# Optimization experiments

Hardware: AMD Instinct MI355X
Metric: run time of the kernel (lower is better)

The kernel has to match this reference:

```python
import jax, jax.numpy as jnp
import numpy as np

B, D, M = 1024, 4096, 128          # batch, input_dim, output_dim (num modules)
HS = [32, 64, 128, 256, 512]       # hidden_dims


def setup_inputs() -> dict:
    key = jax.random.key(0)
    ks = jax.random.split(key, 12)
    inp = {}
    inp["x"] = jax.random.normal(ks[0], (B, D), dtype=jnp.float32)
    # first dense layer: Linear(input_dim, hidden_dims[0]*output_dim)
    inp["W0"] = jax.random.normal(ks[1], (HS[0] * M, D), dtype=jnp.float32) / np.float32(np.sqrt(D))
    inp["b0"] = jnp.zeros((HS[0] * M,), jnp.float32)
    # block-diagonal MaskedLinear layers stored as per-module blocks [M, h_out, h_in]
    for i in range(len(HS) - 1):
        inp[f"W{i+1}"] = jax.random.normal(ks[2 + i], (M, HS[i + 1], HS[i]), dtype=jnp.float32) / np.float32(np.sqrt(HS[i]))
        inp[f"b{i+1}"] = jnp.zeros((M, HS[i + 1]), jnp.float32)
    # output MaskedLinear(h_last, 1, M): blocks [M, 1, h_last] stored as [M, h_last]
    inp["Wout"] = jax.random.normal(ks[10], (M, HS[-1]), dtype=jnp.float32) / np.float32(np.sqrt(HS[-1]))
    inp["bout"] = jnp.zeros((M,), jnp.float32)
    return inp


def reference(x, W0, b0, W1, b1, W2, b2, W3, b3, W4, b4, Wout, bout):
    # Dropout is inference-disabled; MaskedLinear's block-diagonal dense GEMM is
    # computed exactly as a grouped GEMM over the M module blocks (same math,
    # skipping the structurally-zero off-diagonal blocks).
    h = jax.nn.relu(x @ W0.T + b0)                 # [B, M*h0]
    h = h.reshape(x.shape[0], M, HS[0])            # [B, M, h0]
    for W, b in ((W1, b1), (W2, b2), (W3, b3), (W4, b4)):
        h = jax.nn.relu(jnp.einsum('bmi,moi->bmo', h, W) + b)  # [B, M, h_out]
    logits = jnp.einsum('bmi,mi->bm', h, Wout) + bout          # [B, M]
    return jax.nn.sigmoid(logits)
```

## Files before the change

kernel.cpp:

```cpp
#include <hip/hip_runtime.h>
#include <hip/hip_bf16.h>


using bf16 = __hip_bfloat16;
typedef short bf16x8 __attribute__((ext_vector_type(8)));
typedef float f32x4 __attribute__((ext_vector_type(4)));

constexpr int B_ = 1024;
constexpr int M_ = 128;

#define WAITV(N) asm volatile("s_waitcnt vmcnt(" #N ")" ::: "memory")
#define WAITL()  asm volatile("s_waitcnt lgkmcnt(0)" ::: "memory")
#define BAR()    asm volatile("s_barrier" ::: "memory")

__device__ __forceinline__ void gload16_lds(const bf16* gp, bf16* lp) {
    __builtin_amdgcn_global_load_lds(
        (__attribute__((address_space(1))) void*)const_cast<bf16*>(gp),
        (__attribute__((address_space(3))) void*)lp,
        16, 0, 0);
}

struct CvtArgs {
    const float4* src[6];
    short4* dst[6];
};
__global__ void cvt_all(CvtArgs a) {
    constexpr int starts[7] = {0, 1048576, 5242880, 5308416, 5570560,
                               6619136, 10813440};
    int i = blockIdx.x * blockDim.x + threadIdx.x;
    if (i >= starts[6]) return;
    int s = 0;
#pragma unroll
    for (int k = 1; k < 6; ++k) s += (i >= starts[k]) ? 1 : 0;
    int off = i - starts[s];
    float4 v = a.src[s][off];
    union { bf16 h[4]; short4 s4; } u;
    u.h[0] = __float2bfloat16(v.x);
    u.h[1] = __float2bfloat16(v.y);
    u.h[2] = __float2bfloat16(v.z);
    u.h[3] = __float2bfloat16(v.w);
    a.dst[s][off] = u.s4;
}

__global__ __launch_bounds__(256, 2)
void gemm_l0(const bf16* __restrict__ A, const bf16* __restrict__ W,
             const float* __restrict__ bias, bf16* __restrict__ C) {
    constexpr int LDA = 4096;
    __shared__ __align__(16) bf16 sA[2][2][128 * 32];
    __shared__ __align__(16) bf16 sB[2][2][64 * 32];

    const int tid = threadIdx.x, w = tid >> 6, lane = tid & 63;
    const int q = lane >> 4, ln = lane & 15;
    const int lr = lane >> 2, lk = lane & 3;
    const int swz = (lk ^ (lr & 3)) * 8;
    const int wm = w >> 1, wn = w & 1;
    const int r0 = blockIdx.y * 128, c0 = blockIdx.x * 64;

    auto stage = [&](int s, int set) {
        const int k0 = s * 64;
#pragma unroll
        for (int h = 0; h < 2; ++h) {
#pragma unroll
            for (int t = 0; t < 2; ++t) {
                int grp = w * 2 + t;
                gload16_lds(A + (size_t)(r0 + grp * 16 + lr) * LDA + k0 + h * 32 + swz,
                            &sA[set][h][grp * 512]);
            }
            gload16_lds(W + (size_t)(c0 + w * 16 + lr) * LDA + k0 + h * 32 + swz,
                        &sB[set][h][w * 512]);
        }
    };

    f32x4 acc[4][2];
#pragma unroll
    for (int i = 0; i < 4; ++i)
#pragma unroll
        for (int j = 0; j < 2; ++j) acc[i][j] = (f32x4){0.f, 0.f, 0.f, 0.f};

    stage(0, 0);
    stage(1, 1);
    for (int r = 0; r < 64; ++r) {
        if (r < 63) WAITV(6); else WAITV(0);
        BAR();
        const int set = r & 1;
        bf16x8 aF[2][4], bF[2][2];
#pragma unroll
        for (int h = 0; h < 2; ++h) {
#pragma unroll
            for (int i = 0; i < 4; ++i) {
                int row = wm * 64 + i * 16 + ln;
                aF[h][i] = *(const bf16x8*)&sA[set][h][row * 32 + ((q ^ (row & 3)) * 8)];
            }
#pragma unroll
            for (int j = 0; j < 2; ++j) {
                int rn = wn * 32 + j * 16 + ln;
                bF[h][j] = *(const bf16x8*)&sB[set][h][rn * 32 + ((q ^ (rn & 3)) * 8)];
            }
        }
        WAITL();
        BAR();
        if (r + 2 < 64) stage(r + 2, set);
#pragma unroll
        for (int h = 0; h < 2; ++h)
#pragma unroll
            for (int i = 0; i < 4; ++i)
#pragma unroll
                for (int j = 0; j < 2; ++j)
                    acc[i][j] = __builtin_amdgcn_mfma_f32_16x16x32_bf16(
                        aF[h][i], bF[h][j], acc[i][j], 0, 0, 0);
    }

#pragma unroll
    for (int j = 0; j < 2; ++j) {
        int col = c0 + wn * 32 + j * 16 + ln;
        float bv = bias[col];
#pragma unroll
        for (int i = 0; i < 4; ++i)
#pragma unroll
            for (int rr = 0; rr < 4; ++rr) {
                int row = r0 + wm * 64 + i * 16 + q * 4 + rr;
                float v = acc[i][j][rr] + bv;
                v = v > 0.f ? v : 0.f;
                C[(size_t)row * 4096 + col] = __float2bfloat16(v);
            }
    }
}

__global__ __launch_bounds__(256, 2)
void modules_fused(const bf16* __restrict__ h0g,
                   const bf16* __restrict__ W1b, const float* __restrict__ b1,
                   const bf16* __restrict__ W2b, const float* __restrict__ b2,
                   const bf16* __restrict__ W3b, const float* __restrict__ b3,
                   const bf16* __restrict__ W4b, const float* __restrict__ b4,
                   const float* __restrict__ Wout, const float* __restrict__ bout,
                   float* __restrict__ out) {
    constexpr int H3O = 0, H2O = 16896, H1O = 25600, H0O = 30208;
    constexpr int P4B0 = 16896, P4B1 = 20992, P4B2 = 25600;
    __shared__ __align__(16) bf16 pool[32768];

    const int tid = threadIdx.x, w = tid >> 6, lane = tid & 63;
    const int q = lane >> 4, ln = lane & 15;
    const int lr = lane >> 2, lk = lane & 3;
    const int swz = (lk ^ (lr & 3)) * 8;
    const int m = blockIdx.y;
    const int r0 = blockIdx.x * 64;

    const bf16* W1m = W1b + (size_t)m * 64 * 32;
    const bf16* W2m = W2b + (size_t)m * 128 * 64;
    const bf16* W3m = W3b + (size_t)m * 256 * 128;
    const bf16* W4m = W4b + (size_t)m * 512 * 256;

    auto stage = [&](const bf16* G, int ldg, int rows, int nr0, int k0, int woff) {
#pragma unroll
        for (int t = 0; t < rows / 64; ++t) {
            int r = t * 64 + w * 16 + lr;
            gload16_lds(G + (size_t)(nr0 + r) * ldg + k0 + swz,
                        pool + woff + t * 2048 + w * 512);
        }
    };
    auto rdA = [&](int hoff, int stride, int row, int kc) -> bf16x8 {
        return *(const bf16x8*)&pool[hoff + row * stride + kc * 8];
    };
    auto rdA0 = [&](int row) -> bf16x8 {
        return *(const bf16x8*)&pool[H0O + row * 32 + ((q ^ (row & 3)) * 8)];
    };
    auto rdB = [&](int woff, int rn) -> bf16x8 {
        return *(const bf16x8*)&pool[woff + rn * 32 + ((q ^ (rn & 3)) * 8)];
    };
    auto wrH = [&](int hoff, int stride, int row, int col, float v) {
        pool[hoff + row * stride + col] = __float2bfloat16(v);
    };

    float b1v = b1[m * 64 + w * 16 + ln];
    float b2v[2], b3v[4], b4v[4][2], wov[4][2];
#pragma unroll
    for (int j = 0; j < 2; ++j) b2v[j] = b2[m * 128 + w * 32 + j * 16 + ln];
#pragma unroll
    for (int j = 0; j < 4; ++j) b3v[j] = b3[m * 256 + w * 64 + j * 16 + ln];
#pragma unroll
    for (int nc = 0; nc < 4; ++nc)
#pragma unroll
        for (int j = 0; j < 2; ++j) {
            int col = nc * 128 + w * 32 + j * 16 + ln;
            b4v[nc][j] = b4[(size_t)m * 512 + col];
            wov[nc][j] = Wout[(size_t)m * 512 + col];
        }
    float boutv = bout[m];
    WAITV(0);

    gload16_lds(h0g + (size_t)(r0 + w * 16 + lr) * 4096 + m * 32 + swz,
                pool + H0O + w * 512);
    stage(W1m, 32, 64, 0, 0, 8192);
    stage(W2m, 64, 128, 0, 0, 0);
    stage(W2m, 64, 128, 0, 32, 4096);

    WAITV(4);
    BAR();
    {
        bf16x8 aF[4], bF;
#pragma unroll
        for (int i = 0; i < 4; ++i) aF[i] = rdA0(i * 16 + ln);
        bF = rdB(8192, w * 16 + ln);
        WAITL();
        BAR();
        f32x4 a1[4];
#pragma unroll
        for (int i = 0; i < 4; ++i) {
            a1[i] = (f32x4){0.f, 0.f, 0.f, 0.f};
            a1[i] = __builtin_amdgcn_mfma_f32_16x16x32_bf16(aF[i], bF, a1[i], 0, 0, 0);
        }
        int col = w * 16 + ln;
#pragma unroll
        for (int i = 0; i < 4; ++i)
#pragma unroll
            for (int rr = 0; rr < 4; ++rr) {
                float v = a1[i][rr] + b1v;
                v = v > 0.f ? v : 0.f;
                wrH(H1O, 72, i * 16 + q * 4 + rr, col, v);
            }
        WAITL();
        BAR();
    }

    {
        f32x4 a2[4][2];
#pragma unroll
        for (int i = 0; i < 4; ++i)
#pragma unroll
            for (int j = 0; j < 2; ++j) a2[i][j] = (f32x4){0.f, 0.f, 0.f, 0.f};
#pragma unroll
        for (int kr = 0; kr < 2; ++kr) {
            if (kr == 0) WAITV(2); else WAITV(0);
            BAR();
            bf16x8 aF[4], bF[2];
#pragma unroll
            for (int i = 0; i < 4; ++i) aF[i] = rdA(H1O, 72, i * 16 + ln, kr * 4 + q);
#pragma unroll
            for (int j = 0; j < 2; ++j) bF[j] = rdB(kr * 4096, w * 32 + j * 16 + ln);
            WAITL();
            BAR();
            if (kr == 1) {
                stage(W3m, 128, 256, 0, 0, 0);
                stage(W3m, 128, 256, 0, 32, 8192);
            }
#pragma unroll
            for (int i = 0; i < 4; ++i)
#pragma unroll
                for (int j = 0; j < 2; ++j)
                    a2[i][j] = __builtin_amdgcn_mfma_f32_16x16x32_bf16(aF[i], bF[j], a2[i][j], 0, 0, 0);
        }
#pragma unroll
        for (int j = 0; j < 2; ++j) {
            int col = w * 32 + j * 16 + ln;
#pragma unroll
            for (int i = 0; i < 4; ++i)
#pragma unroll
                for (int rr = 0; rr < 4; ++rr) {
                    float v = a2[i][j][rr] + b2v[j];
                    v = v > 0.f ? v : 0.f;
                    wrH(H2O, 136, i * 16 + q * 4 + rr, col, v);
                }
        }
        WAITL();
        BAR();
    }

    {
        f32x4 a3[4][4];
#pragma unroll
        for (int i = 0; i < 4; ++i)
#pragma unroll
            for (int j = 0; j < 4; ++j) a3[i][j] = (f32x4){0.f, 0.f, 0.f, 0.f};
#pragma unroll
        for (int kr = 0; kr < 4; ++kr) {
            if (kr < 3) WAITV(4); else WAITV(0);
            BAR();
            bf16x8 aF[4], bF[4];
#pragma unroll
            for (int i = 0; i < 4; ++i) aF[i] = rdA(H2O, 136, i * 16 + ln, kr * 4 + q);
#pragma unroll
            for (int j = 0; j < 4; ++j) bF[j] = rdB((kr & 1) * 8192, w * 64 + j * 16 + ln);
            WAITL();
            BAR();
            if (kr == 0)      stage(W3m, 128, 256, 0, 64, 0);
            else if (kr == 1) stage(W3m, 128, 256, 0, 96, 8192);
            else if (kr == 3) {
                stage(W4m, 256, 128, 0, 0, P4B0);
                stage(W4m, 256, 128, 0, 32, P4B1);
            }
#pragma unroll
            for (int i = 0; i < 4; ++i)
#pragma unroll
                for (int j = 0; j < 4; ++j)
                    a3[i][j] = __builtin_amdgcn_mfma_f32_16x16x32_bf16(aF[i], bF[j], a3[i][j], 0, 0, 0);
        }
#pragma unroll
        for (int j = 0; j < 4; ++j) {
            int col = w * 64 + j * 16 + ln;
#pragma unroll
            for (int i = 0; i < 4; ++i)
#pragma unroll
                for (int rr = 0; rr < 4; ++rr) {
                    float v = a3[i][j][rr] + b3v[j];
                    v = v > 0.f ? v : 0.f;
                    wrH(H3O, 264, i * 16 + q * 4 + rr, col, v);
                }
        }
        WAITL();
        BAR();
    }

    float pl[4][4];
#pragma unroll
    for (int i = 0; i < 4; ++i)
#pragma unroll
        for (int rr = 0; rr < 4; ++rr) pl[i][rr] = 0.f;

#pragma unroll
    for (int nc = 0; nc < 4; ++nc) {
        f32x4 a4[4][2];
#pragma unroll
        for (int i = 0; i < 4; ++i)
#pragma unroll
            for (int j = 0; j < 2; ++j) a4[i][j] = (f32x4){0.f, 0.f, 0.f, 0.f};
#pragma unroll
        for (int kr = 0; kr < 8; ++kr) {
            const int r = nc * 8 + kr;
            if (r + 2 < 32) {
                const int r2 = r + 2;
                const int wb2 = (r2 % 3 == 0) ? P4B0 : (r2 % 3 == 1) ? P4B1 : P4B2;
                stage(W4m, 256, 128, (r2 >> 3) * 128, (r2 & 7) * 32, wb2);
            }
            if (r < 30) WAITV(4); else if (r == 30) WAITV(2); else WAITV(0);
            BAR();
            const int wb = (r % 3 == 0) ? P4B0 : (r % 3 == 1) ? P4B1 : P4B2;
            bf16x8 aF[4], bF[2];
#pragma unroll
            for (int i = 0; i < 4; ++i) aF[i] = rdA(H3O, 264, i * 16 + ln, kr * 4 + q);
#pragma unroll
            for (int j = 0; j < 2; ++j) bF[j] = rdB(wb, w * 32 + j * 16 + ln);
            WAITL();
            BAR();
#pragma unroll
            for (int i = 0; i < 4; ++i)
#pragma unroll
                for (int j = 0; j < 2; ++j)
                    a4[i][j] = __builtin_amdgcn_mfma_f32_16x16x32_bf16(aF[i], bF[j], a4[i][j], 0, 0, 0);
        }
#pragma unroll
        for (int j = 0; j < 2; ++j) {
            float bb = b4v[nc][j], wv = wov[nc][j];
#pragma unroll
            for (int i = 0; i < 4; ++i)
#pragma unroll
                for (int rr = 0; rr < 4; ++rr) {
                    float v = a4[i][j][rr] + bb;
                    v = v > 0.f ? v : 0.f;
                    pl[i][rr] += v * wv;
                }
        }
    }

    float* sc = (float*)&pool[H0O];
#pragma unroll
    for (int i = 0; i < 4; ++i)
#pragma unroll
        for (int rr = 0; rr < 4; ++rr) {
            float p = pl[i][rr];
            p += __shfl_xor(p, 1);
            p += __shfl_xor(p, 2);
            p += __shfl_xor(p, 4);
            p += __shfl_xor(p, 8);
            if (ln == 0) sc[w * 64 + i * 16 + q * 4 + rr] = p;
        }
    __syncthreads();
    if (tid < 64) {
        float s = sc[tid] + sc[64 + tid] + sc[128 + tid] + sc[192 + tid];
        float lg = s + boutv;
        out[(size_t)(r0 + tid) * M_ + m] = 1.f / (1.f + __expf(-lg));
    }
}

extern "C" void kernel_launch(void* const* d_in, const int* in_sizes, int n_in,
                              void* d_out, int out_size, void* d_ws, size_t ws_size,
                              hipStream_t stream) {
    const float* x    = (const float*)d_in[0];
    const float* W0   = (const float*)d_in[1];
    const float* b0   = (const float*)d_in[2];
    const float* W1   = (const float*)d_in[3];
    const float* b1   = (const float*)d_in[4];
    const float* W2   = (const float*)d_in[5];
    const float* b2   = (const float*)d_in[6];
    const float* W3   = (const float*)d_in[7];
    const float* b3   = (const float*)d_in[8];
    const float* W4   = (const float*)d_in[9];
    const float* b4   = (const float*)d_in[10];
    const float* Wout = (const float*)d_in[11];
    const float* bout = (const float*)d_in[12];
    float* out = (float*)d_out;

    char* ws = (char*)d_ws;
    size_t off = 0;
    auto alloc = [&](size_t bytes) -> void* {
        off = (off + 255) & ~(size_t)255;
        void* p = ws + off;
        off += bytes;
        return p;
    };
    bf16* W0b = (bf16*)alloc((size_t)4096 * 4096 * 2);
    bf16* W1b = (bf16*)alloc((size_t)M_ * 64 * 32 * 2);
    bf16* W2b = (bf16*)alloc((size_t)M_ * 128 * 64 * 2);
    bf16* W3b = (bf16*)alloc((size_t)M_ * 256 * 128 * 2);
    bf16* W4b = (bf16*)alloc((size_t)M_ * 512 * 256 * 2);
    bf16* xb  = (bf16*)alloc((size_t)B_ * 4096 * 2);
    bf16* h0  = (bf16*)alloc((size_t)B_ * 4096 * 2);

    CvtArgs ca;
    ca.src[0] = (const float4*)x;  ca.dst[0] = (short4*)xb;
    ca.src[1] = (const float4*)W0; ca.dst[1] = (short4*)W0b;
    ca.src[2] = (const float4*)W1; ca.dst[2] = (short4*)W1b;
    ca.src[3] = (const float4*)W2; ca.dst[3] = (short4*)W2b;
    ca.src[4] = (const float4*)W3; ca.dst[4] = (short4*)W3b;
    ca.src[5] = (const float4*)W4; ca.dst[5] = (short4*)W4b;
    cvt_all<<<(10813440 + 255) / 256, 256, 0, stream>>>(ca);

    {
        dim3 g(4096 / 64, B_ / 128, 1);
        gemm_l0<<<g, 256, 0, stream>>>(xb, W0b, b0, h0);
    }
    {
        dim3 g(B_ / 64, M_, 1);
        modules_fused<<<g, 256, 0, stream>>>(h0, W1b, b1, W2b, b2, W3b, b3,
                                             W4b, b4, Wout, bout, out);
    }
}
```

Before: 321.9 us.

## Load module weights directly into registers and shrink LDS for higher occupancy

Weight fragments for layers 1-4 are now loaded from global memory straight into registers with a two-deep register prefetch, replacing the LDS staging and its per-step barriers. Activations stay in LDS with an XOR swizzle in place of padded strides, and the layer-3 output is computed in two column halves. These changes cut LDS from 64KB to 48KB and raise launch bounds to 3 blocks per CU. The aim is fewer barriers and more resident waves, at the cost of uncoalesced per-lane global weight loads, more register pressure, and exposed global latency.

```diff
diff --git a/kernel.cpp b/kernel.cpp
--- a/kernel.cpp
+++ b/kernel.cpp
@@ -126,7 +126,7 @@
     }
 }
 
-__global__ __launch_bounds__(256, 2)
+__global__ __launch_bounds__(256, 3)
 void modules_fused(const bf16* __restrict__ h0g,
                    const bf16* __restrict__ W1b, const float* __restrict__ b1,
                    const bf16* __restrict__ W2b, const float* __restrict__ b2,
@@ -134,9 +134,8 @@
                    const bf16* __restrict__ W4b, const float* __restrict__ b4,
                    const float* __restrict__ Wout, const float* __restrict__ bout,
                    float* __restrict__ out) {
-    constexpr int H3O = 0, H2O = 16896, H1O = 25600, H0O = 30208;
-    constexpr int P4B0 = 16896, P4B1 = 20992, P4B2 = 25600;
-    __shared__ __align__(16) bf16 pool[32768];
+    constexpr int H3 = 0, H1 = 0, H0 = 4096, H2 = 16384;
+    __shared__ __align__(16) bf16 pool[24576];
 
     const int tid = threadIdx.x, w = tid >> 6, lane = tid & 63;
     const int q = lane >> 4, ln = lane & 15;
@@ -150,33 +149,29 @@
     const bf16* W3m = W3b + (size_t)m * 256 * 128;
     const bf16* W4m = W4b + (size_t)m * 512 * 256;
 
-    auto stage = [&](const bf16* G, int ldg, int rows, int nr0, int k0, int woff) {
-#pragma unroll
-        for (int t = 0; t < rows / 64; ++t) {
-            int r = t * 64 + w * 16 + lr;
-            gload16_lds(G + (size_t)(nr0 + r) * ldg + k0 + swz,
-                        pool + woff + t * 2048 + w * 512);
-        }
-    };
-    auto rdA = [&](int hoff, int stride, int row, int kc) -> bf16x8 {
-        return *(const bf16x8*)&pool[hoff + row * stride + kc * 8];
+    auto rdX = [&](int base, int nch, int row, int chunk) -> bf16x8 {
+        return *(const bf16x8*)&pool[base + row * nch * 8 + ((chunk ^ (row & 7)) * 8)];
     };
     auto rdA0 = [&](int row) -> bf16x8 {
-        return *(const bf16x8*)&pool[H0O + row * 32 + ((q ^ (row & 3)) * 8)];
-    };
-    auto rdB = [&](int woff, int rn) -> bf16x8 {
-        return *(const bf16x8*)&pool[woff + rn * 32 + ((q ^ (rn & 3)) * 8)];
-    };
-    auto wrH = [&](int hoff, int stride, int row, int col, float v) {
-        pool[hoff + row * stride + col] = __float2bfloat16(v);
+        return *(const bf16x8*)&pool[H0 + row * 32 + ((q ^ (row & 3)) * 8)];
+    };
+    auto wrX = [&](int base, int nch, int row, int col, float v) {
+        pool[base + row * nch * 8 + (((col >> 3) ^ (row & 7)) * 8) + (col & 7)] =
+            __float2bfloat16(v);
+    };
+    auto ldW = [&](const bf16* Wm, int ldg, int row, int kc) -> bf16x8 {
+        return *(const bf16x8*)&Wm[(size_t)row * ldg + kc * 8];
     };
 
     float b1v = b1[m * 64 + w * 16 + ln];
-    float b2v[2], b3v[4], b4v[4][2], wov[4][2];
+    float b2v[2], b3v[2][2], b4v[4][2], wov[4][2];
 #pragma unroll
     for (int j = 0; j < 2; ++j) b2v[j] = b2[m * 128 + w * 32 + j * 16 + ln];
 #pragma unroll
-    for (int j = 0; j < 4; ++j) b3v[j] = b3[m * 256 + w * 64 + j * 16 + ln];
+    for (int oc = 0; oc < 2; ++oc)
+#pragma unroll
+        for (int j = 0; j < 2; ++j)
+            b3v[oc][j] = b3[m * 256 + oc * 128 + w * 32 + j * 16 + ln];
 #pragma unroll
     for (int nc = 0; nc < 4; ++nc)
 #pragma unroll
@@ -186,129 +181,123 @@
             wov[nc][j] = Wout[(size_t)m * 512 + col];
         }
     float boutv = bout[m];
+
+    gload16_lds(h0g + (size_t)(r0 + w * 16 + lr) * 4096 + m * 32 + swz,
+                pool + H0 + w * 512);
+    bf16x8 f1 = ldW(W1m, 32, w * 16 + ln, q);
+    bf16x8 f2[2][2], f3[2][2], f4[2][2];
+#pragma unroll
+    for (int kk = 0; kk < 2; ++kk)
+#pragma unroll
+        for (int j = 0; j < 2; ++j)
+            f2[kk][j] = ldW(W2m, 64, w * 32 + j * 16 + ln, kk * 4 + q);
+#pragma unroll
+    for (int p = 0; p < 2; ++p)
+#pragma unroll
+        for (int j = 0; j < 2; ++j)
+            f3[p][j] = ldW(W3m, 128, w * 32 + j * 16 + ln, p * 4 + q);
     WAITV(0);
-
-    gload16_lds(h0g + (size_t)(r0 + w * 16 + lr) * 4096 + m * 32 + swz,
-                pool + H0O + w * 512);
-    stage(W1m, 32, 64, 0, 0, 8192);
-    stage(W2m, 64, 128, 0, 0, 0);
-    stage(W2m, 64, 128, 0, 32, 4096);
-
-    WAITV(4);
     BAR();
+
     {
-        bf16x8 aF[4], bF;
-#pragma unroll
-        for (int i = 0; i < 4; ++i) aF[i] = rdA0(i * 16 + ln);
-        bF = rdB(8192, w * 16 + ln);
+        f32x4 a1[4];
+#pragma unroll
+        for (int i = 0; i < 4; ++i) {
+            a1[i] = (f32x4){0.f, 0.f, 0.f, 0.f};
+            a1[i] = __builtin_amdgcn_mfma_f32_16x16x32_bf16(rdA0(i * 16 + ln), f1,
+                                                            a1[i], 0, 0, 0);
+        }
+#pragma unroll
+        for (int i = 0; i < 4; ++i)
+#pragma unroll
+            for (int rr = 0; rr < 4; ++rr) {
+                float v = a1[i][rr] + b1v;
+                wrX(H1, 8, i * 16 + q * 4 + rr, w * 16 + ln, v > 0.f ? v : 0.f);
+            }
         WAITL();
         BAR();
-        f32x4 a1[4];
-#pragma unroll
-        for (int i = 0; i < 4; ++i) {
-            a1[i] = (f32x4){0.f, 0.f, 0.f, 0.f};
-            a1[i] = __builtin_amdgcn_mfma_f32_16x16x32_bf16(aF[i], bF, a1[i], 0, 0, 0);
-        }
-        int col = w * 16 + ln;
+    }
+
+    {
+        f32x4 a2[4][2];
 #pragma unroll
         for (int i = 0; i < 4; ++i)
 #pragma unroll
-            for (int rr = 0; rr < 4; ++rr) {
-                float v = a1[i][rr] + b1v;
-                v = v > 0.f ? v : 0.f;
-                wrH(H1O, 72, i * 16 + q * 4 + rr, col, v);
-            }
+            for (int j = 0; j < 2; ++j) a2[i][j] = (f32x4){0.f, 0.f, 0.f, 0.f};
+#pragma unroll
+        for (int kk = 0; kk < 2; ++kk) {
+            bf16x8 aF[4];
+#pragma unroll
+            for (int i = 0; i < 4; ++i) aF[i] = rdX(H1, 8, i * 16 + ln, kk * 4 + q);
+#pragma unroll
+            for (int i = 0; i < 4; ++i)
+#pragma unroll
+                for (int j = 0; j < 2; ++j)
+                    a2[i][j] = __builtin_amdgcn_mfma_f32_16x16x32_bf16(
+                        aF[i], f2[kk][j], a2[i][j], 0, 0, 0);
+        }
+#pragma unroll
+        for (int j = 0; j < 2; ++j)
+#pragma unroll
+            for (int i = 0; i < 4; ++i)
+#pragma unroll
+                for (int rr = 0; rr < 4; ++rr) {
+                    float v = a2[i][j][rr] + b2v[j];
+                    wrX(H2, 16, i * 16 + q * 4 + rr, w * 32 + j * 16 + ln,
+                        v > 0.f ? v : 0.f);
+                }
         WAITL();
         BAR();
     }
 
-    {
-        f32x4 a2[4][2];
+#pragma unroll
+    for (int oc = 0; oc < 2; ++oc) {
+        f32x4 a3[4][2];
 #pragma unroll
         for (int i = 0; i < 4; ++i)
 #pragma unroll
-            for (int j = 0; j < 2; ++j) a2[i][j] = (f32x4){0.f, 0.f, 0.f, 0.f};
-#pragma unroll
-        for (int kr = 0; kr < 2; ++kr) {
-            if (kr == 0) WAITV(2); else WAITV(0);
-            BAR();
-            bf16x8 aF[4], bF[2];
-#pragma unroll
-            for (int i = 0; i < 4; ++i) aF[i] = rdA(H1O, 72, i * 16 + ln, kr * 4 + q);
-#pragma unroll
-            for (int j = 0; j < 2; ++j) bF[j] = rdB(kr * 4096, w * 32 + j * 16 + ln);
-            WAITL();
-            BAR();
-            if (kr == 1) {
-                stage(W3m, 128, 256, 0, 0, 0);
-                stage(W3m, 128, 256, 0, 32, 8192);
-            }
+            for (int j = 0; j < 2; ++j) a3[i][j] = (f32x4){0.f, 0.f, 0.f, 0.f};
+#pragma unroll
+        for (int kr = 0; kr < 4; ++kr) {
+            const int r = oc * 4 + kr, p = r & 1;
+            bf16x8 c0 = f3[p][0], c1 = f3[p][1];
+            if (r + 2 < 8) {
+                const int r2 = r + 2;
+#pragma unroll
+                for (int j = 0; j < 2; ++j)
+                    f3[p][j] = ldW(W3m, 128,
+                                   (r2 >> 2) * 128 + w * 32 + j * 16 + ln,
+                                   (r2 & 3) * 4 + q);
+            }
+            bf16x8 aF[4];
+#pragma unroll
+            for (int i = 0; i < 4; ++i) aF[i] = rdX(H2, 16, i * 16 + ln, kr * 4 + q);
+#pragma unroll
+            for (int i = 0; i < 4; ++i) {
+                a3[i][0] = __builtin_amdgcn_mfma_f32_16x16x32_bf16(aF[i], c0,
+                                                                   a3[i][0], 0, 0, 0);
+                a3[i][1] = __builtin_amdgcn_mfma_f32_16x16x32_bf16(aF[i], c1,
+                                                                   a3[i][1], 0, 0, 0);
+            }
+        }
+#pragma unroll
+        for (int j = 0; j < 2; ++j)
 #pragma unroll
             for (int i = 0; i < 4; ++i)
 #pragma unroll
-                for (int j = 0; j < 2; ++j)
-                    a2[i][j] = __builtin_amdgcn_mfma_f32_16x16x32_bf16(aF[i], bF[j], a2[i][j], 0, 0, 0);
-        }
-#pragma unroll
-        for (int j = 0; j < 2; ++j) {
-            int col = w * 32 + j * 16 + ln;
-#pragma unroll
-            for (int i = 0; i < 4; ++i)
-#pragma unroll
                 for (int rr = 0; rr < 4; ++rr) {
-                    float v = a2[i][j][rr] + b2v[j];
-                    v = v > 0.f ? v : 0.f;
-                    wrH(H2O, 136, i * 16 + q * 4 + rr, col, v);
+                    float v = a3[i][j][rr] + b3v[oc][j];
+                    wrX(H3, 32, i * 16 + q * 4 + rr,
+                        oc * 128 + w * 32 + j * 16 + ln, v > 0.f ? v : 0.f);
                 }
-        }
-        WAITL();
-        BAR();
-    }
-
-    {
-        f32x4 a3[4][4];
-#pragma unroll
-        for (int i = 0; i < 4; ++i)
-#pragma unroll
-            for (int j = 0; j < 4; ++j) a3[i][j] = (f32x4){0.f, 0.f, 0.f, 0.f};
-#pragma unroll
-        for (int kr = 0; kr < 4; ++kr) {
-            if (kr < 3) WAITV(4); else WAITV(0);
-            BAR();
-            bf16x8 aF[4], bF[4];
-#pragma unroll
-            for (int i = 0; i < 4; ++i) aF[i] = rdA(H2O, 136, i * 16 + ln, kr * 4 + q);
-#pragma unroll
-            for (int j = 0; j < 4; ++j) bF[j] = rdB((kr & 1) * 8192, w * 64 + j * 16 + ln);
-            WAITL();
-            BAR();
-            if (kr == 0)      stage(W3m, 128, 256, 0, 64, 0);
-            else if (kr == 1) stage(W3m, 128, 256, 0, 96, 8192);
-            else if (kr == 3) {
-                stage(W4m, 256, 128, 0, 0, P4B0);
-                stage(W4m, 256, 128, 0, 32, P4B1);
-            }
-#pragma unroll
-            for (int i = 0; i < 4; ++i)
-#pragma unroll
-                for (int j = 0; j < 4; ++j)
-                    a3[i][j] = __builtin_amdgcn_mfma_f32_16x16x32_bf16(aF[i], bF[j], a3[i][j], 0, 0, 0);
-        }
-#pragma unroll
-        for (int j = 0; j < 4; ++j) {
-            int col = w * 64 + j * 16 + ln;
-#pragma unroll
-            for (int i = 0; i < 4; ++i)
-#pragma unroll
-                for (int rr = 0; rr < 4; ++rr) {
-                    float v = a3[i][j][rr] + b3v[j];
-                    v = v > 0.f ? v : 0.f;
-                    wrH(H3O, 264, i * 16 + q * 4 + rr, col, v);
-                }
-        }
-        WAITL();
-        BAR();
-    }
+    }
+#pragma unroll
+    for (int p = 0; p < 2; ++p)
+#pragma unroll
+        for (int j = 0; j < 2; ++j)
+            f4[p][j] = ldW(W4m, 256, w * 32 + j * 16 + ln, p * 4 + q);
+    WAITL();
+    BAR();
 
     float pl[4][4];
 #pragma unroll
@@ -325,27 +314,26 @@
             for (int j = 0; j < 2; ++j) a4[i][j] = (f32x4){0.f, 0.f, 0.f, 0.f};
 #pragma unroll
         for (int kr = 0; kr < 8; ++kr) {
-            const int r = nc * 8 + kr;
+            const int r = nc * 8 + kr, p = r & 1;
+            bf16x8 c0 = f4[p][0], c1 = f4[p][1];
             if (r + 2 < 32) {
                 const int r2 = r + 2;
-                const int wb2 = (r2 % 3 == 0) ? P4B0 : (r2 % 3 == 1) ? P4B1 : P4B2;
-                stage(W4m, 256, 128, (r2 >> 3) * 128, (r2 & 7) * 32, wb2);
-            }
-            if (r < 30) WAITV(4); else if (r == 30) WAITV(2); else WAITV(0);
-            BAR();
-            const int wb = (r % 3 == 0) ? P4B0 : (r % 3 == 1) ? P4B1 : P4B2;
-            bf16x8 aF[4], bF[2];
-#pragma unroll
-            for (int i = 0; i < 4; ++i) aF[i] = rdA(H3O, 264, i * 16 + ln, kr * 4 + q);
-#pragma unroll
-            for (int j = 0; j < 2; ++j) bF[j] = rdB(wb, w * 32 + j * 16 + ln);
-            WAITL();
-            BAR();
-#pragma unroll
-            for (int i = 0; i < 4; ++i)
 #pragma unroll
                 for (int j = 0; j < 2; ++j)
-                    a4[i][j] = __builtin_amdgcn_mfma_f32_16x16x32_bf16(aF[i], bF[j], a4[i][j], 0, 0, 0);
+                    f4[p][j] = ldW(W4m, 256,
+                                   (r2 >> 3) * 128 + w * 32 + j * 16 + ln,
+                                   (r2 & 7) * 4 + q);
+            }
+            bf16x8 aF[4];
+#pragma unroll
+            for (int i = 0; i < 4; ++i) aF[i] = rdX(H3, 32, i * 16 + ln, kr * 4 + q);
+#pragma unroll
+            for (int i = 0; i < 4; ++i) {
+                a4[i][0] = __builtin_amdgcn_mfma_f32_16x16x32_bf16(aF[i], c0,
+                                                                   a4[i][0], 0, 0, 0);
+                a4[i][1] = __builtin_amdgcn_mfma_f32_16x16x32_bf16(aF[i], c1,
+                                                                   a4[i][1], 0, 0, 0);
+            }
         }
 #pragma unroll
         for (int j = 0; j < 2; ++j) {
@@ -361,7 +349,7 @@
         }
     }
 
-    float* sc = (float*)&pool[H0O];
+    float* sc = (float*)&pool[H2];
 #pragma unroll
     for (int i = 0; i < 4; ++i)
 #pragma unroll
```

After: 432.7 us. 1.34x slower.

## Shrink LDS footprint with XOR-swizzled H3 and double-buffered W4 staging

Applied to the files above, without the earlier changes.

Cuts the fused module kernel's shared-memory pool from 64 KB to about 49 KB. It does this by storing the layer-3 activations with an XOR swizzle instead of padded rows, overlaying buffers, and dropping from triple- to double-buffered W4 tile staging. The aim is to let more workgroups fit per CU and to avoid LDS bank conflicts without padding. The cost is a shorter prefetch distance: each refill is issued only after the previous tile has been read, which can expose more global-load latency.

```diff
diff --git a/kernel.cpp b/kernel.cpp
--- a/kernel.cpp
+++ b/kernel.cpp
@@ -134,9 +134,14 @@
                    const bf16* __restrict__ W4b, const float* __restrict__ b4,
                    const float* __restrict__ Wout, const float* __restrict__ bout,
                    float* __restrict__ out) {
-    constexpr int H3O = 0, H2O = 16896, H1O = 25600, H0O = 30208;
-    constexpr int P4B0 = 16896, P4B1 = 20992, P4B2 = 25600;
-    __shared__ __align__(16) bf16 pool[32768];
+    constexpr int H3O = 0;
+    constexpr int W1B = 8192;
+    constexpr int H1O = 10240;
+    constexpr int H0O = 16384;
+    constexpr int H2O = 16384;
+    constexpr int P4B0 = 16384, P4B1 = 20480;
+    constexpr int SCO = 24576;
+    __shared__ __align__(16) bf16 pool[25088];
 
     const int tid = threadIdx.x, w = tid >> 6, lane = tid & 63;
     const int q = lane >> 4, ln = lane & 15;
@@ -170,6 +175,13 @@
     auto wrH = [&](int hoff, int stride, int row, int col, float v) {
         pool[hoff + row * stride + col] = __float2bfloat16(v);
     };
+    auto wrH3 = [&](int row, int col, float v) {
+        pool[H3O + row * 256 + (((col >> 3) ^ (row & 7)) * 8) + (col & 7)] =
+            __float2bfloat16(v);
+    };
+    auto rdA3 = [&](int row, int kc) -> bf16x8 {
+        return *(const bf16x8*)&pool[H3O + row * 256 + ((kc ^ (row & 7)) * 8)];
+    };
 
     float b1v = b1[m * 64 + w * 16 + ln];
     float b2v[2], b3v[4], b4v[4][2], wov[4][2];
@@ -190,7 +202,7 @@
 
     gload16_lds(h0g + (size_t)(r0 + w * 16 + lr) * 4096 + m * 32 + swz,
                 pool + H0O + w * 512);
-    stage(W1m, 32, 64, 0, 0, 8192);
+    stage(W1m, 32, 64, 0, 0, W1B);
     stage(W2m, 64, 128, 0, 0, 0);
     stage(W2m, 64, 128, 0, 32, 4096);
 
@@ -200,7 +212,7 @@
         bf16x8 aF[4], bF;
 #pragma unroll
         for (int i = 0; i < 4; ++i) aF[i] = rdA0(i * 16 + ln);
-        bF = rdB(8192, w * 16 + ln);
+        bF = rdB(W1B, w * 16 + ln);
         WAITL();
         BAR();
         f32x4 a1[4];
@@ -303,7 +315,7 @@
                 for (int rr = 0; rr < 4; ++rr) {
                     float v = a3[i][j][rr] + b3v[j];
                     v = v > 0.f ? v : 0.f;
-                    wrH(H3O, 264, i * 16 + q * 4 + rr, col, v);
+                    wrH3(i * 16 + q * 4 + rr, col, v);
                 }
         }
         WAITL();
@@ -326,21 +338,20 @@
 #pragma unroll
         for (int kr = 0; kr < 8; ++kr) {
             const int r = nc * 8 + kr;
+            if (r < 31) WAITV(2); else WAITV(0);
+            BAR();
+            const int wb = (r & 1) ? P4B1 : P4B0;
+            bf16x8 aF[4], bF[2];
+#pragma unroll
+            for (int i = 0; i < 4; ++i) aF[i] = rdA3(i * 16 + ln, kr * 4 + q);
+#pragma unroll
+            for (int j = 0; j < 2; ++j) bF[j] = rdB(wb, w * 32 + j * 16 + ln);
+            WAITL();
+            BAR();
             if (r + 2 < 32) {
                 const int r2 = r + 2;
-                const int wb2 = (r2 % 3 == 0) ? P4B0 : (r2 % 3 == 1) ? P4B1 : P4B2;
-                stage(W4m, 256, 128, (r2 >> 3) * 128, (r2 & 7) * 32, wb2);
-            }
-            if (r < 30) WAITV(4); else if (r == 30) WAITV(2); else WAITV(0);
-            BAR();
-            const int wb = (r % 3 == 0) ? P4B0 : (r % 3 == 1) ? P4B1 : P4B2;
-            bf16x8 aF[4], bF[2];
-#pragma unroll
-            for (int i = 0; i < 4; ++i) aF[i] = rdA(H3O, 264, i * 16 + ln, kr * 4 + q);
-#pragma unroll
-            for (int j = 0; j < 2; ++j) bF[j] = rdB(wb, w * 32 + j * 16 + ln);
-            WAITL();
-            BAR();
+                stage(W4m, 256, 128, (r2 >> 3) * 128, (r2 & 7) * 32, wb);
+            }
 #pragma unroll
             for (int i = 0; i < 4; ++i)
 #pragma unroll
@@ -361,7 +372,7 @@
         }
     }
 
-    float* sc = (float*)&pool[H0O];
+    float* sc = (float*)&pool[SCO];
 #pragma unroll
     for (int i = 0; i < 4; ++i)
 #pragma unroll
```

Measured after the change: 328.9 us. 1.02x slower.
